# Kernel tuning notes

Hardware: AMD Instinct MI355X
Metric: run time of the kernel (lower is better)

The kernel has to match this reference:

```python
import jax, jax.numpy as jnp
import numpy as np

B, C, H, W = 4, 64, 256, 256
KH = KW = 3
K = KH * KW
HO, WO = H - 2, W - 2  # VALID 3x3 conv output


def conv2d_valid(x, w, b):
    y = jax.lax.conv_general_dilated(x, w, (1, 1), 'VALID',
                                     dimension_numbers=('NCHW', 'OIHW', 'NCHW'))
    return y + b[None, :, None, None]


def bilinear_gather(x, py, px):
    # x: [B,C,H,W]; py, px: [B,K,HO,WO] fractional sample coords (zero outside).
    y0 = jnp.floor(py)
    x0 = jnp.floor(px)
    ly = py - y0
    lx = px - x0
    y0i = y0.astype(jnp.int32)
    x0i = x0.astype(jnp.int32)
    xf = x.reshape(B, C, H * W)

    def g(yi, xi):
        valid = (yi >= 0) & (yi < H) & (xi >= 0) & (xi < W)
        idx = jnp.clip(yi, 0, H - 1) * W + jnp.clip(xi, 0, W - 1)
        idxf = idx.reshape(B, -1)
        out = jax.vmap(lambda xb, ib: xb[:, ib])(xf, idxf)  # [B,C,K*HO*WO]
        out = out.reshape(B, C, K, HO, WO)
        return out * valid[:, None].astype(x.dtype)

    v = (((1 - ly) * (1 - lx))[:, None] * g(y0i, x0i)
         + ((1 - ly) * lx)[:, None] * g(y0i, x0i + 1)
         + (ly * (1 - lx))[:, None] * g(y0i + 1, x0i)
         + (ly * lx)[:, None] * g(y0i + 1, x0i + 1))
    return v  # [B,C,K,HO,WO]


def deform_conv(x, offset, w, b):
    # offset: [B, 2*K, HO, WO] with channel pairs (dy_k, dx_k), k row-major over 3x3.
    off = offset.reshape(B, K, 2, HO, WO)
    dy, dx = off[:, :, 0], off[:, :, 1]
    kh = (jnp.arange(K) // KW).astype(jnp.float32)
    kw = (jnp.arange(K) % KW).astype(jnp.float32)
    py = jnp.arange(HO, dtype=jnp.float32)[None, None, :, None] + kh[None, :, None, None] + dy
    px = jnp.arange(WO, dtype=jnp.float32)[None, None, None, :] + kw[None, :, None, None] + dx
    s = bilinear_gather(x, py, px)  # [B,C,K,HO,WO]
    out = jnp.einsum('bckhw,ock->bohw', s, w.reshape(w.shape[0], C, K))
    return out + b[None, :, None, None]


def setup_inputs() -> dict:
    key = jax.random.key(0)
    k1, k2, k3 = jax.random.split(key, 3)
    fan = C * KH * KW
    x = jax.random.normal(k1, (B, C, H, W), jnp.float32)
    offset_w = jax.random.normal(k2, (2 * K, C, KH, KW), jnp.float32) * 0.01
    offset_b = jnp.zeros((2 * K,), jnp.float32)
    deform_w = jax.random.normal(k3, (1, C, KH, KW), jnp.float32) * (1.0 / np.sqrt(fan))
    deform_b = jnp.zeros((1,), jnp.float32)
    return {'x': x, 'offset_w': offset_w, 'offset_b': offset_b,
            'deform_w': deform_w, 'deform_b': deform_b}


def reference(x, offset_w, offset_b, deform_w, deform_b):
    offset = conv2d_valid(x, offset_w, offset_b)  # [B,18,HO,WO]
    return deform_conv(x, offset, deform_w, deform_b)  # [B,1,HO,WO]
```

## Files before the change

### kernel.cpp

```cpp
#include <hip/hip_runtime.h>
#include <hip/hip_bf16.h>

#define BB 4
#define CC 64
#define HH 256
#define WW 256
#define KK 9
#define NOFF 18
#define HO 254
#define WO 254
#define NPIX (HO*WO)

typedef __attribute__((ext_vector_type(8))) short bf16x8;
typedef __attribute__((ext_vector_type(4))) float f32x4;

__device__ __align__(16) unsigned char  g_wpack[23552];
__device__ __align__(16) unsigned short g_xT[(size_t)BB * 2 * HH * WW * 32];

#define GLB(p)  ((const __attribute__((address_space(1))) void*)(p))
#define LDSP(p) ((__attribute__((address_space(3))) void*)(p))

static __device__ __forceinline__ unsigned short f2bf(float v) {
    __hip_bfloat16 h = __float2bfloat16(v);
    union { __hip_bfloat16 b; unsigned short u; } cv; cv.b = h; return cv.u;
}
static __device__ __forceinline__ float bf2f(unsigned short u) {
    unsigned int w = ((unsigned int)u) << 16;
    float f; __builtin_memcpy(&f, &w, 4); return f;
}

static __device__ __forceinline__ void repack_piece(
    int tap, int tid, int nthr,
    const float* __restrict__ offset_w,
    const float* __restrict__ deform_w)
{
    if (tap < 9) {
        for (int i = tid; i < 18 * 64; i += nthr) {
            int o = i >> 6;
            int c = i & 63;
            int row = tap * 18 + o;
            unsigned int byte = (unsigned)(row * 128 + c * 2) ^ (((unsigned)(row & 7)) << 4);
            *(unsigned short*)(g_wpack + byte) = f2bf(offset_w[((size_t)o * CC + c) * KK + tap]);
        }
    } else {
        for (int i = tid; i < 16 * 64; i += nthr) {
            int t = i >> 6;
            int c = i & 63;
            float v = (t < KK) ? deform_w[(size_t)c * KK + t] : 0.0f;
            unsigned int byte = (unsigned)(t * 128 + c * 2) ^ (((unsigned)(t & 7)) << 4);
            *(unsigned short*)(g_wpack + 20736 + byte) = f2bf(v);
        }
    }
}

__global__ __launch_bounds__(256) void transpose_kernel(
    const float* __restrict__ x,
    const float* __restrict__ offset_w,
    const float* __restrict__ deform_w)
{
    __shared__ float s[64][65];
    const int tid = threadIdx.x;
    const int w0 = blockIdx.x * 64;
    const int h  = blockIdx.y;
    const int b  = blockIdx.z;

    if (b == 0 && blockIdx.x == 0 && h < 10)
        repack_piece(h, tid, 256, offset_w, deform_w);

    #pragma unroll
    for (int it = 0; it < 4; ++it) {
        int i  = tid + it * 256;
        int c  = i >> 4;
        int p4 = (i & 15) << 2;
        float4 v = *(const float4*)(x + (((size_t)b * CC + c) * HH + h) * WW + w0 + p4);
        s[c][p4 + 0] = v.x; s[c][p4 + 1] = v.y; s[c][p4 + 2] = v.z; s[c][p4 + 3] = v.w;
    }
    __syncthreads();
    #pragma unroll
    for (int it = 0; it < 2; ++it) {
        int j  = tid + it * 256;
        int px = j >> 3;
        int g  = j & 7;
        unsigned int u[4];
        #pragma unroll
        for (int q = 0; q < 4; ++q) {
            __hip_bfloat162 h2 = __float22bfloat162_rn(
                make_float2(s[g * 8 + 2 * q][px], s[g * 8 + 2 * q + 1][px]));
            __builtin_memcpy(&u[q], &h2, 4);
        }
        const int half = g >> 2;
        unsigned short* dst = g_xT
            + ((size_t)(b * 2 + half) * HH * WW + (size_t)h * WW + w0 + px) * 32 + (g & 3) * 8;
        *(uint4*)dst = make_uint4(u[0], u[1], u[2], u[3]);
    }
}

#define PTF 22
#define NCF 484
#define ROWB 1408
#define PATCHB (22*ROWB)
#define LDS_WP 0
#define LDS_PATCH 23552
#define SMEM_F (23552 + PATCHB)
#define LDS_SOFF 0
#define LDS_SY   18504

__global__ __launch_bounds__(256) void conv_gather_fused(
    const float* __restrict__ offset_b,
    const float* __restrict__ deform_w,
    const float* __restrict__ deform_b,
    float* __restrict__ out)
{
    __shared__ __align__(16) unsigned char smem[SMEM_F];
    const int tid = threadIdx.x;
    const int wv = tid >> 6;
    const int l  = tid & 63;
    const int lr = l & 15;
    const int lk = l >> 4;

    const int x0 = blockIdx.x * 16;
    const int y0 = blockIdx.y * 16;
    const int b  = blockIdx.z;

    for (int j = wv; j < 23; j += 4) {
        if (j * 64 + l < 1424)
            __builtin_amdgcn_global_load_lds(GLB(g_wpack + (size_t)j * 1024 + l * 16),
                                             LDSP(smem + LDS_WP + j * 1024), 16, 0, 0);
    }

    auto stage_half = [&](int h) {
        const unsigned char* hb = (const unsigned char*)(g_xT + (size_t)(b * 2 + h) * HH * WW * 32);
        for (int r = wv; r < 22; r += 4) {
            const int gy = min(max(y0 - 2 + r, 0), HH - 1);
            const unsigned char* rowbase = hb + (size_t)gy * WW * 64;
            #pragma unroll
            for (int q = 0; q < 2; ++q) {
                const int pl = q * 1024 + (l << 4);
                if (pl < ROWB) {
                    unsigned p = (unsigned)(r * ROWB + pl);
                    unsigned s = (p ^ (((p >> 7) & 7u) << 4)) - (unsigned)(r * ROWB);
                    const int cell   = (int)(s >> 6);
                    const int within = (int)(s & 63u);
                    const int gx = min(max(x0 - 2 + cell, 0), WW - 1);
                    __builtin_amdgcn_global_load_lds(GLB(rowbase + ((size_t)gx << 6) + within),
                                                     LDSP(smem + LDS_PATCH + r * ROWB + q * 1024),
                                                     16, 0, 0);
                }
            }
        }
    };

    const int o1 = (16 + lr > 17) ? 17 : 16 + lr;
    const float bias0 = offset_b[lr];
    const float bias1 = (lr < 2) ? offset_b[16 + lr] : 0.0f;

    f32x4 accC[4][2];
    f32x4 accY[8];
    #pragma unroll
    for (int mi = 0; mi < 4; ++mi)
        #pragma unroll
        for (int reg = 0; reg < 4; ++reg) { accC[mi][0][reg] = bias0; accC[mi][1][reg] = bias1; }
    #pragma unroll
    for (int j = 0; j < 8; ++j) accY[j] = (f32x4){0.f, 0.f, 0.f, 0.f};

    auto ldw = [&](int row, int cbyte) -> bf16x8 {
        unsigned int byte = (unsigned)(row * 128 + cbyte) ^ (((unsigned)(row & 7)) << 4);
        return *(const bf16x8*)(smem + LDS_WP + byte);
    };
    auto lda = [&](int cell) -> bf16x8 {
        unsigned lin = (unsigned)(cell * 64 + lk * 16);
        lin ^= ((lin >> 7) & 7u) << 4;
        return *(const bf16x8*)(smem + LDS_PATCH + lin);
    };

    auto mfma_half = [&](int h) {
        const int cbyte = h * 64 + lk * 16;
        #pragma unroll
        for (int kw = 0; kw < 3; ++kw) {
            #pragma unroll
            for (int kh = 0; kh < 3; ++kh) {
                const int tap = kh * 3 + kw;
                bf16x8 b0 = ldw(tap * 18 + lr, cbyte);
                bf16x8 b1 = ldw(tap * 18 + o1, cbyte);
                #pragma unroll
                for (int mi = 0; mi < 4; ++mi) {
                    const int cell = (4 * wv + mi + kh + 2) * PTF + (lr + kw + 2);
                    bf16x8 a = lda(cell);
                    accC[mi][0] = __builtin_amdgcn_mfma_f32_16x16x32_bf16(a, b0, accC[mi][0], 0, 0, 0);
                    accC[mi][1] = __builtin_amdgcn_mfma_f32_16x16x32_bf16(a, b1, accC[mi][1], 0, 0, 0);
                }
            }
        }
        {
            unsigned int byY = (unsigned)(lr * 128 + cbyte) ^ (((unsigned)(lr & 7)) << 4);
            bf16x8 bY = *(const bf16x8*)(smem + LDS_WP + 20736 + byY);
            #pragma unroll
            for (int j = 0; j < 8; ++j) {
                const int t = wv + 4 * j;
                if (t < 31) {
                    int cell = t * 16 + lr; if (cell > NCF - 1) cell = NCF - 1;
                    bf16x8 a = lda(cell);
                    accY[j] = __builtin_amdgcn_mfma_f32_16x16x32_bf16(a, bY, accY[j], 0, 0, 0);
                }
            }
        }
    };

    stage_half(0);
    __syncthreads();
    mfma_half(0);
    __syncthreads();
    stage_half(1);
    __syncthreads();
    mfma_half(1);
    __syncthreads();

    float* s_off = (float*)(smem + LDS_SOFF);
    float* s_Y   = (float*)(smem + LDS_SY);
    #pragma unroll
    for (int mi = 0; mi < 4; ++mi) {
        #pragma unroll
        for (int nt = 0; nt < 2; ++nt) {
            const int o = nt * 16 + lr;
            if (o < NOFF) {
                const int pbase = (4 * wv + mi) * 16 + lk * 4;
                #pragma unroll
                for (int reg = 0; reg < 4; ++reg)
                    s_off[o * 257 + pbase + reg] = accC[mi][nt][reg];
            }
        }
    }
    #pragma unroll
    for (int j = 0; j < 8; ++j) {
        const int t = wv + 4 * j;
        if (t < 31 && lr < KK) {
            #pragma unroll
            for (int reg = 0; reg < 4; ++reg) {
                const int cell = t * 16 + lk * 4 + reg;
                if (cell < NCF) {
                    int r = cell / PTF, col = cell - r * PTF;
                    int gy = y0 - 2 + r, gx = x0 - 2 + col;
                    bool inimg = (gy >= 0 && gy < HH && gx >= 0 && gx < WW);
                    s_Y[lr * 485 + cell] = inimg ? accY[j][reg] : 0.0f;
                }
            }
        }
    }
    __syncthreads();

    const int ty = tid >> 4, tx = tid & 15;
    const int ho = y0 + ty, wo = x0 + tx;
    if (ho >= HO || wo >= WO) return;

    float acc = deform_b[0];

    #pragma unroll
    for (int k = 0; k < KK; ++k) {
        const int kh = k / 3, kw = k % 3;
        float dy = s_off[(2 * k) * 257 + tid];
        float dx = s_off[(2 * k + 1) * 257 + tid];
        float py = (float)(ho + kh) + dy;
        float px = (float)(wo + kw) + dx;
        float y0f = floorf(py), x0f = floorf(px);
        float ly = py - y0f, lx = px - x0f;
        int yi0 = (int)y0f, xi0 = (int)x0f;
        int ry = yi0 - (y0 - 2);
        int rx = xi0 - (x0 - 2);
        float w00 = (1.0f - ly) * (1.0f - lx);
        float w01 = (1.0f - ly) * lx;
        float w10 = ly * (1.0f - lx);
        float w11 = ly * lx;
        float g;
        if ((unsigned)ry <= (unsigned)(PTF - 2) && (unsigned)rx <= (unsigned)(PTF - 2)) {
            const float* tp = s_Y + k * 485;
            const int id = ry * PTF + rx;
            g = w00 * tp[id]       + w01 * tp[id + 1]
              + w10 * tp[id + PTF] + w11 * tp[id + PTF + 1];
        } else {
            int yi1 = yi0 + 1, xi1 = xi0 + 1;
            float m00 = (yi0 >= 0 && yi0 < HH && xi0 >= 0 && xi0 < WW) ? w00 : 0.0f;
            float m01 = (yi0 >= 0 && yi0 < HH && xi1 >= 0 && xi1 < WW) ? w01 : 0.0f;
            float m10 = (yi1 >= 0 && yi1 < HH && xi0 >= 0 && xi0 < WW) ? w10 : 0.0f;
            float m11 = (yi1 >= 0 && yi1 < HH && xi1 >= 0 && xi1 < WW) ? w11 : 0.0f;
            int y0c = min(max(yi0, 0), HH - 1), y1c = min(max(yi1, 0), HH - 1);
            int x0c = min(max(xi0, 0), WW - 1), x1c = min(max(xi1, 0), WW - 1);
            g = 0.0f;
            #pragma unroll
            for (int h = 0; h < 2; ++h) {
                const unsigned short* xh = g_xT + (size_t)(b * 2 + h) * HH * WW * 32;
                const unsigned short* p00 = xh + (size_t)(y0c * WW + x0c) * 32;
                const unsigned short* p01 = xh + (size_t)(y0c * WW + x1c) * 32;
                const unsigned short* p10 = xh + (size_t)(y1c * WW + x0c) * 32;
                const unsigned short* p11 = xh + (size_t)(y1c * WW + x1c) * 32;
                for (int c = 0; c < 32; ++c) {
                    float gc = m00 * bf2f(p00[c]) + m01 * bf2f(p01[c])
                             + m10 * bf2f(p10[c]) + m11 * bf2f(p11[c]);
                    g = fmaf(gc, deform_w[(size_t)(h * 32 + c) * KK + k], g);
                }
            }
        }
        acc += g;
    }

    out[(size_t)b * NPIX + ho * WO + wo] = acc;
}

extern "C" void kernel_launch(void* const* d_in, const int* in_sizes, int n_in,
                              void* d_out, int out_size, void* d_ws, size_t ws_size,
                              hipStream_t stream) {
    const float* x        = (const float*)d_in[0];
    const float* offset_w = (const float*)d_in[1];
    const float* offset_b = (const float*)d_in[2];
    const float* deform_w = (const float*)d_in[3];
    const float* deform_b = (const float*)d_in[4];
    float* out = (float*)d_out;

    hipLaunchKernelGGL(transpose_kernel, dim3(4, 256, BB), dim3(256), 0, stream,
                       x, offset_w, deform_w);
    hipLaunchKernelGGL(conv_gather_fused, dim3(16, 16, BB), dim3(256), 0, stream,
                       offset_b, deform_w, deform_b, out);
}
```

Before: 41.47 us.

## Shrink patch halo to one pixel and stage both channel halves together

The input patch per block shrinks from 22x22 to 20x20 cells, since the offset conv and the 3x3 gather window only need a one-pixel halo. Both channel halves are now loaded into separate LDS buffers up front, with a single barrier, instead of alternating stage/compute with four barriers. The per-tap Y projection MFMAs drop from 8 to 7 tile groups. This raises LDS use per block and narrows the in-LDS fast path for the bilinear gather, so more samples may fall back to global loads when offsets are large.

```diff
diff --git a/kernel.cpp b/kernel.cpp
--- a/kernel.cpp
+++ b/kernel.cpp
@@ -95,13 +95,14 @@
     }
 }
 
-#define PTF 22
-#define NCF 484
-#define ROWB 1408
-#define PATCHB (22*ROWB)
+#define PTF 20
+#define NCF 400
+#define ROWB 1280
+#define PATCHB (20*ROWB)
 #define LDS_WP 0
-#define LDS_PATCH 23552
-#define SMEM_F (23552 + PATCHB)
+#define LDS_P0 23552
+#define LDS_P1 (23552 + PATCHB)
+#define SMEM_F (23552 + 2*PATCHB)
 #define LDS_SOFF 0
 #define LDS_SY   18504
 
@@ -122,58 +123,55 @@
     const int y0 = blockIdx.y * 16;
     const int b  = blockIdx.z;
 
-    for (int j = wv; j < 23; j += 4) {
-        if (j * 64 + l < 1424)
-            __builtin_amdgcn_global_load_lds(GLB(g_wpack + (size_t)j * 1024 + l * 16),
-                                             LDSP(smem + LDS_WP + j * 1024), 16, 0, 0);
-    }
-
-    auto stage_half = [&](int h) {
+    for (int k = wv; k < 23; k += 4)
+        __builtin_amdgcn_global_load_lds(GLB(g_wpack + (size_t)k * 1024 + l * 16),
+                                         LDSP(smem + LDS_WP + k * 1024), 16, 0, 0);
+
+    auto stage_half = [&](int h, int ldsbase) {
         const unsigned char* hb = (const unsigned char*)(g_xT + (size_t)(b * 2 + h) * HH * WW * 32);
-        for (int r = wv; r < 22; r += 4) {
-            const int gy = min(max(y0 - 2 + r, 0), HH - 1);
-            const unsigned char* rowbase = hb + (size_t)gy * WW * 64;
-            #pragma unroll
-            for (int q = 0; q < 2; ++q) {
-                const int pl = q * 1024 + (l << 4);
-                if (pl < ROWB) {
-                    unsigned p = (unsigned)(r * ROWB + pl);
-                    unsigned s = (p ^ (((p >> 7) & 7u) << 4)) - (unsigned)(r * ROWB);
-                    const int cell   = (int)(s >> 6);
-                    const int within = (int)(s & 63u);
-                    const int gx = min(max(x0 - 2 + cell, 0), WW - 1);
-                    __builtin_amdgcn_global_load_lds(GLB(rowbase + ((size_t)gx << 6) + within),
-                                                     LDSP(smem + LDS_PATCH + r * ROWB + q * 1024),
-                                                     16, 0, 0);
-                }
-            }
+        for (int k = wv; k < 25; k += 4) {
+            unsigned p = (unsigned)(k * 1024 + (l << 4));
+            unsigned s = p ^ (((p >> 7) & 7u) << 4);
+            int r    = (int)(s / (unsigned)ROWB);
+            int pl   = (int)(s % (unsigned)ROWB);
+            int cell = pl >> 6;
+            int within = pl & 63;
+            int gy = min(max(y0 - 1 + r, 0), HH - 1);
+            int gx = min(max(x0 - 1 + cell, 0), WW - 1);
+            __builtin_amdgcn_global_load_lds(GLB(hb + ((size_t)gy * WW + gx) * 64 + within),
+                                             LDSP(smem + ldsbase + k * 1024), 16, 0, 0);
         }
     };
+    stage_half(0, LDS_P0);
+    stage_half(1, LDS_P1);
+    __syncthreads();
 
     const int o1 = (16 + lr > 17) ? 17 : 16 + lr;
     const float bias0 = offset_b[lr];
     const float bias1 = (lr < 2) ? offset_b[16 + lr] : 0.0f;
 
     f32x4 accC[4][2];
-    f32x4 accY[8];
+    f32x4 accY[7];
     #pragma unroll
     for (int mi = 0; mi < 4; ++mi)
         #pragma unroll
         for (int reg = 0; reg < 4; ++reg) { accC[mi][0][reg] = bias0; accC[mi][1][reg] = bias1; }
     #pragma unroll
-    for (int j = 0; j < 8; ++j) accY[j] = (f32x4){0.f, 0.f, 0.f, 0.f};
+    for (int j = 0; j < 7; ++j) accY[j] = (f32x4){0.f, 0.f, 0.f, 0.f};
 
     auto ldw = [&](int row, int cbyte) -> bf16x8 {
         unsigned int byte = (unsigned)(row * 128 + cbyte) ^ (((unsigned)(row & 7)) << 4);
         return *(const bf16x8*)(smem + LDS_WP + byte);
     };
-    auto lda = [&](int cell) -> bf16x8 {
+    auto lda = [&](int ldsbase, int cell) -> bf16x8 {
         unsigned lin = (unsigned)(cell * 64 + lk * 16);
         lin ^= ((lin >> 7) & 7u) << 4;
-        return *(const bf16x8*)(smem + LDS_PATCH + lin);
+        return *(const bf16x8*)(smem + ldsbase + lin);
     };
 
-    auto mfma_half = [&](int h) {
+    #pragma unroll
+    for (int h = 0; h < 2; ++h) {
+        const int pbase_lds = h ? LDS_P1 : LDS_P0;
         const int cbyte = h * 64 + lk * 16;
         #pragma unroll
         for (int kw = 0; kw < 3; ++kw) {
@@ -184,8 +182,8 @@
                 bf16x8 b1 = ldw(tap * 18 + o1, cbyte);
                 #pragma unroll
                 for (int mi = 0; mi < 4; ++mi) {
-                    const int cell = (4 * wv + mi + kh + 2) * PTF + (lr + kw + 2);
-                    bf16x8 a = lda(cell);
+                    const int cell = (4 * wv + mi + kh + 1) * PTF + (lr + kw + 1);
+                    bf16x8 a = lda(pbase_lds, cell);
                     accC[mi][0] = __builtin_amdgcn_mfma_f32_16x16x32_bf16(a, b0, accC[mi][0], 0, 0, 0);
                     accC[mi][1] = __builtin_amdgcn_mfma_f32_16x16x32_bf16(a, b1, accC[mi][1], 0, 0, 0);
                 }
@@ -195,24 +193,16 @@
             unsigned int byY = (unsigned)(lr * 128 + cbyte) ^ (((unsigned)(lr & 7)) << 4);
             bf16x8 bY = *(const bf16x8*)(smem + LDS_WP + 20736 + byY);
             #pragma unroll
-            for (int j = 0; j < 8; ++j) {
+            for (int j = 0; j < 7; ++j) {
                 const int t = wv + 4 * j;
-                if (t < 31) {
-                    int cell = t * 16 + lr; if (cell > NCF - 1) cell = NCF - 1;
-                    bf16x8 a = lda(cell);
+                if (t < 25) {
+                    bf16x8 a = lda(pbase_lds, t * 16 + lr);
                     accY[j] = __builtin_amdgcn_mfma_f32_16x16x32_bf16(a, bY, accY[j], 0, 0, 0);
                 }
             }
         }
-    };
-
-    stage_half(0);
-    __syncthreads();
-    mfma_half(0);
-    __syncthreads();
-    stage_half(1);
-    __syncthreads();
-    mfma_half(1);
+    }
+
     __syncthreads();
 
     float* s_off = (float*)(smem + LDS_SOFF);
@@ -231,18 +221,16 @@
         }
     }
     #pragma unroll
-    for (int j = 0; j < 8; ++j) {
+    for (int j = 0; j < 7; ++j) {
         const int t = wv + 4 * j;
-        if (t < 31 && lr < KK) {
+        if (t < 25 && lr < KK) {
             #pragma unroll
             for (int reg = 0; reg < 4; ++reg) {
                 const int cell = t * 16 + lk * 4 + reg;
-                if (cell < NCF) {
-                    int r = cell / PTF, col = cell - r * PTF;
-                    int gy = y0 - 2 + r, gx = x0 - 2 + col;
-                    bool inimg = (gy >= 0 && gy < HH && gx >= 0 && gx < WW);
-                    s_Y[lr * 485 + cell] = inimg ? accY[j][reg] : 0.0f;
-                }
+                int r = cell / PTF, col = cell - r * PTF;
+                int gy = y0 - 1 + r, gx = x0 - 1 + col;
+                bool inimg = (gy >= 0 && gy < HH && gx >= 0 && gx < WW);
+                s_Y[lr * 401 + cell] = inimg ? accY[j][reg] : 0.0f;
             }
         }
     }
@@ -264,15 +252,15 @@
         float y0f = floorf(py), x0f = floorf(px);
         float ly = py - y0f, lx = px - x0f;
         int yi0 = (int)y0f, xi0 = (int)x0f;
-        int ry = yi0 - (y0 - 2);
-        int rx = xi0 - (x0 - 2);
+        int ry = yi0 - (y0 - 1);
+        int rx = xi0 - (x0 - 1);
         float w00 = (1.0f - ly) * (1.0f - lx);
         float w01 = (1.0f - ly) * lx;
         float w10 = ly * (1.0f - lx);
         float w11 = ly * lx;
         float g;
         if ((unsigned)ry <= (unsigned)(PTF - 2) && (unsigned)rx <= (unsigned)(PTF - 2)) {
-            const float* tp = s_Y + k * 485;
+            const float* tp = s_Y + k * 401;
             const int id = ry * PTF + rx;
             g = w00 * tp[id]       + w01 * tp[id + 1]
               + w10 * tp[id + PTF] + w11 * tp[id + PTF + 1];
```

Result: slower. 42.98 us (+3.6%).
